# Performance work log

Measured on AMD Instinct MI355X. Metric: run time of the kernel, lower is better.

The kernel has to match this reference:

```python
import jax, jax.numpy as jnp
import numpy as np

D = 1024
B, S = 4, 2048

def setup_inputs() -> dict:
    key = jax.random.key(0)
    ks = jax.random.split(key, 9)
    scale = 1.0 / np.sqrt(D)
    return {
        "queries": jax.random.normal(ks[0], (B, S, D), dtype=jnp.float32),
        "keys": jax.random.normal(ks[1], (B, S, D), dtype=jnp.float32),
        "values": jax.random.normal(ks[2], (B, S, D), dtype=jnp.float32),
        # torch nn.Linear weights: [out, in], y = x @ W.T + b
        "Wq": jax.random.uniform(ks[3], (D, D), jnp.float32, -scale, scale),
        "bq": jax.random.uniform(ks[4], (D,), jnp.float32, -scale, scale),
        "Wk": jax.random.uniform(ks[5], (D, D), jnp.float32, -scale, scale),
        "bk": jax.random.uniform(ks[6], (D,), jnp.float32, -scale, scale),
        "Wv": jax.random.uniform(ks[7], (D, D), jnp.float32, -scale, scale),
        "bv": jax.random.uniform(ks[8], (D,), jnp.float32, -scale, scale),
    }

def reference(queries, keys, values, Wq, bq, Wk, bk, Wv, bv):
    # Linear projections (torch convention: x @ W.T + b)
    Q = jnp.einsum('bsd,ed->bse', queries, Wq) + bq  # [B,S,D]
    K = jnp.einsum('bsd,ed->bse', keys, Wk) + bk
    V = jnp.einsum('bsd,ed->bse', values, Wv) + bv
    # relu attention: no softmax, no scaling (faithful to source)
    scores = jax.nn.relu(jnp.einsum('bqd,bkd->bqk', Q, K))  # [B,S,S]
    return jnp.einsum('bqk,bkd->bqd', scores, V)
```

## Files before the change

### kernel.cpp

```cpp
#include <hip/hip_runtime.h>
#include <hip/hip_bf16.h>
#include <stdint.h>

typedef __bf16 bf16_t;
typedef __bf16 bf16x8 __attribute__((ext_vector_type(8)));
typedef float f32x4 __attribute__((ext_vector_type(4)));

#define TILE 128
#define BK 32

__device__ __forceinline__ void async_copy16(const bf16_t* g, bf16_t* l) {
    __builtin_amdgcn_global_load_lds(
        (const __attribute__((address_space(1))) unsigned int*)(uintptr_t)g,
        (__attribute__((address_space(3))) unsigned int*)(uintptr_t)l,
        16, 0, 0);
}

template<bool OUT_F32, bool RELU, int BIAS_MODE>
__global__ __launch_bounds__(256, 2)
void gemm_bt(const bf16_t* __restrict__ A, const bf16_t* __restrict__ B,
             const float* __restrict__ bias, void* __restrict__ Cp,
             int K, int ldc, long sAb, long sBb, long sCb)
{
    __shared__ bf16_t As[TILE * BK];
    __shared__ bf16_t Bs[TILE * BK];

    const int b      = blockIdx.z;
    const int blockM = blockIdx.y * TILE;
    const int blockN = blockIdx.x * TILE;
    const int t      = threadIdx.x;
    const int lane   = t & 63;
    const int wave   = t >> 6;
    const int wm     = (wave >> 1) * 64;
    const int wn     = (wave & 1) * 64;
    const int fr     = lane & 15;
    const int fk     = (lane >> 4) * 8;
    const int quad   = lane >> 4;

    f32x4 acc[4][4] = {};

    const bf16_t* Ab = A + sAb * (long)b;
    const bf16_t* Bb = B + sBb * (long)b;

    const int c0 = t, c1 = t + 256;
    const int r0 = c0 >> 2, e0 = (c0 & 3) * 8;
    const int r1 = c1 >> 2, e1 = (c1 & 3) * 8;
    const bf16_t* a0 = Ab + (long)(blockM + r0) * K + e0;
    const bf16_t* a1 = Ab + (long)(blockM + r1) * K + e1;
    const bf16_t* b0 = Bb + (long)(blockN + r0) * K + e0;
    const bf16_t* b1 = Bb + (long)(blockN + r1) * K + e1;
    bf16_t* lA0 = &As[c0 * 8]; bf16_t* lA1 = &As[c1 * 8];
    bf16_t* lB0 = &Bs[c0 * 8]; bf16_t* lB1 = &Bs[c1 * 8];

    for (int k0 = 0; k0 < K; k0 += BK) {
        async_copy16(a0 + k0, lA0);
        async_copy16(a1 + k0, lA1);
        async_copy16(b0 + k0, lB0);
        async_copy16(b1 + k0, lB1);
        __syncthreads();

        bf16x8 afr[4], bfr[4];
        #pragma unroll
        for (int i = 0; i < 4; i++)
            afr[i] = *(const bf16x8*)&As[(wm + i*16 + fr) * BK + fk];
        #pragma unroll
        for (int j = 0; j < 4; j++)
            bfr[j] = *(const bf16x8*)&Bs[(wn + j*16 + fr) * BK + fk];

        #pragma unroll
        for (int i = 0; i < 4; i++)
            #pragma unroll
            for (int j = 0; j < 4; j++)
                acc[i][j] = __builtin_amdgcn_mfma_f32_16x16x32_bf16(
                                afr[i], bfr[j], acc[i][j], 0, 0, 0);
        __syncthreads();
    }

    float*  Cf = (float*) Cp + sCb * (long)b;
    bf16_t* Ch = (bf16_t*)Cp + sCb * (long)b;
    #pragma unroll
    for (int i = 0; i < 4; i++) {
        #pragma unroll
        for (int j = 0; j < 4; j++) {
            const int gcol = blockN + wn + j*16 + fr;
            float bcol = 0.f;
            if (BIAS_MODE == 1) bcol = bias[gcol];
            #pragma unroll
            for (int r = 0; r < 4; r++) {
                const int grow = blockM + wm + i*16 + quad*4 + r;
                float vv = acc[i][j][r];
                if (BIAS_MODE == 1) vv += bcol;
                if (BIAS_MODE == 2) vv += bias[grow];
                if (RELU) vv = fmaxf(vv, 0.f);
                if (OUT_F32) Cf[(long)grow * ldc + gcol] = vv;
                else         Ch[(long)grow * ldc + gcol] = (bf16_t)vv;
            }
        }
    }
}

__global__ __launch_bounds__(256)
void cast_all_kernel(const float* __restrict__ q, const float* __restrict__ k,
                     const float* __restrict__ v, const float* __restrict__ Wq,
                     const float* __restrict__ Wk, const float* __restrict__ Wv,
                     bf16_t* __restrict__ ws)
{
    const long BIG = 1048576;
    const long SMALL = 131072;
    long id = (long)blockIdx.x * blockDim.x + threadIdx.x;
    const float* src; bf16_t* dst;
    if (id < 3 * BIG) {
        int s = (int)(id / BIG);
        long off = (id - (long)s * BIG) * 8;
        src = (s == 0 ? q : s == 1 ? k : v) + off;
        dst = ws + (long)s * 8388608 + off;
    } else {
        long id2 = id - 3 * BIG;
        int s = (int)(id2 / SMALL);
        long off = (id2 - (long)s * SMALL) * 8;
        src = (s == 0 ? Wq : s == 1 ? Wk : Wv) + off;
        dst = ws + 25165824L + (long)s * 1048576 + off;
    }
    float4 v0 = ((const float4*)src)[0];
    float4 v1 = ((const float4*)src)[1];
    alignas(16) bf16_t o[8];
    o[0]=(bf16_t)v0.x; o[1]=(bf16_t)v0.y; o[2]=(bf16_t)v0.z; o[3]=(bf16_t)v0.w;
    o[4]=(bf16_t)v1.x; o[5]=(bf16_t)v1.y; o[6]=(bf16_t)v1.z; o[7]=(bf16_t)v1.w;
    *(uint4*)dst = *(const uint4*)o;
}

extern "C" void kernel_launch(void* const* d_in, const int* in_sizes, int n_in,
                              void* d_out, int out_size, void* d_ws, size_t ws_size,
                              hipStream_t stream)
{
    const float* q   = (const float*)d_in[0];
    const float* k   = (const float*)d_in[1];
    const float* v   = (const float*)d_in[2];
    const float* Wq  = (const float*)d_in[3];
    const float* bq  = (const float*)d_in[4];
    const float* Wk  = (const float*)d_in[5];
    const float* bk  = (const float*)d_in[6];
    const float* Wv  = (const float*)d_in[7];
    const float* bv  = (const float*)d_in[8];

    const int B = 4, S = 2048, D = 1024;
    const int BS = B * S;

    bf16_t* ws  = (bf16_t*)d_ws;
    bf16_t* qb  = ws;
    bf16_t* kb  = ws + 8388608L;
    bf16_t* vb  = ws + 16777216L;
    bf16_t* Wqb = ws + 25165824L;
    bf16_t* Wkb = ws + 26214400L;
    bf16_t* Wvb = ws + 27262976L;
    bf16_t* Qp  = ws + 28311552L;
    bf16_t* Kp  = ws + 36700160L;
    bf16_t* VpT = ws + 45088768L;
    bf16_t* Sc  = ws;

    dim3 blk(256);

    cast_all_kernel<<<dim3(13824), blk, 0, stream>>>(q, k, v, Wq, Wk, Wv, ws);

    gemm_bt<false, false, 1><<<dim3(D / TILE, BS / TILE, 1), blk, 0, stream>>>(
        qb, Wqb, bq, Qp, D, D, 0L, 0L, 0L);

    gemm_bt<false, false, 1><<<dim3(D / TILE, BS / TILE, 1), blk, 0, stream>>>(
        kb, Wkb, bk, Kp, D, D, 0L, 0L, 0L);

    gemm_bt<false, false, 2><<<dim3(S / TILE, D / TILE, B), blk, 0, stream>>>(
        Wvb, vb, bv, VpT, D, S, 0L, (long)S * D, (long)D * S);

    gemm_bt<false, true, 0><<<dim3(S / TILE, S / TILE, B), blk, 0, stream>>>(
        Qp, Kp, nullptr, Sc, D, S, (long)S * D, (long)S * D, (long)S * S);

    gemm_bt<false  || true, false, 0><<<dim3(D / TILE, S / TILE, B), blk, 0, stream>>>(
        Sc, VpT, nullptr, d_out, S, D, (long)S * S, (long)D * S, (long)S * D);
}
```

Measured before the change: 332.5 us.

## Use 32x32x16 MFMA, BK=64 with XOR-swizzled LDS, and grouped block order

Rewrites the GEMM inner loop to use 32x32x16 bf16 MFMAs instead of 16x16x32, raising the K tile to 64. LDS chunks are stored with an XOR swizzle to avoid bank conflicts on fragment reads. Block indices are remapped into strips of four column blocks for better L2 reuse. Halving the syncs per K and using larger MFMAs should cut LDS traffic and barrier overhead, at the cost of doubled LDS per block (32 KB), which may reduce occupancy.

```diff
diff --git a/kernel.cpp b/kernel.cpp
--- a/kernel.cpp
+++ b/kernel.cpp
@@ -4,10 +4,10 @@
 
 typedef __bf16 bf16_t;
 typedef __bf16 bf16x8 __attribute__((ext_vector_type(8)));
-typedef float f32x4 __attribute__((ext_vector_type(4)));
+typedef float f32x16 __attribute__((ext_vector_type(16)));
 
 #define TILE 128
-#define BK 32
+#define BK 64
 
 __device__ __forceinline__ void async_copy16(const bf16_t* g, bf16_t* l) {
     __builtin_amdgcn_global_load_lds(
@@ -25,71 +25,90 @@
     __shared__ bf16_t As[TILE * BK];
     __shared__ bf16_t Bs[TILE * BK];
 
-    const int b      = blockIdx.z;
-    const int blockM = blockIdx.y * TILE;
-    const int blockN = blockIdx.x * TILE;
-    const int t      = threadIdx.x;
-    const int lane   = t & 63;
-    const int wave   = t >> 6;
-    const int wm     = (wave >> 1) * 64;
-    const int wn     = (wave & 1) * 64;
-    const int fr     = lane & 15;
-    const int fk     = (lane >> 4) * 8;
-    const int quad   = lane >> 4;
+    const int b  = blockIdx.z;
+    const int nb = gridDim.x, mb = gridDim.y;
+    const int SW = 4;
+    int bid   = blockIdx.y * nb + blockIdx.x;
+    int strip = bid / (mb * SW);
+    int rem   = bid - strip * (mb * SW);
+    int bm    = rem / SW;
+    int bn    = strip * SW + (rem - bm * SW);
+    const int blockM = bm * TILE;
+    const int blockN = bn * TILE;
 
-    f32x4 acc[4][4] = {};
+    const int t    = threadIdx.x;
+    const int lane = t & 63;
+    const int wave = t >> 6;
+    const int wm   = (wave >> 1) * 64;
+    const int wn   = (wave & 1) * 64;
+    const int r32  = lane & 31;
+    const int half = lane >> 5;
+    const int kx   = r32 & 7;
+
+    f32x16 acc[2][2] = {};
 
     const bf16_t* Ab = A + sAb * (long)b;
     const bf16_t* Bb = B + sBb * (long)b;
 
-    const int c0 = t, c1 = t + 256;
-    const int r0 = c0 >> 2, e0 = (c0 & 3) * 8;
-    const int r1 = c1 >> 2, e1 = (c1 & 3) * 8;
-    const bf16_t* a0 = Ab + (long)(blockM + r0) * K + e0;
-    const bf16_t* a1 = Ab + (long)(blockM + r1) * K + e1;
-    const bf16_t* b0 = Bb + (long)(blockN + r0) * K + e0;
-    const bf16_t* b1 = Bb + (long)(blockN + r1) * K + e1;
-    bf16_t* lA0 = &As[c0 * 8]; bf16_t* lA1 = &As[c1 * 8];
-    bf16_t* lB0 = &Bs[c0 * 8]; bf16_t* lB1 = &Bs[c1 * 8];
+    const bf16_t* gA[4]; const bf16_t* gB[4];
+    bf16_t* lA[4]; bf16_t* lB[4];
+    #pragma unroll
+    for (int j = 0; j < 4; j++) {
+        int c   = t + j * 256;
+        int row = c >> 3;
+        int kcl = (c & 7) ^ (row & 7);
+        gA[j] = Ab + (long)(blockM + row) * K + kcl * 8;
+        gB[j] = Bb + (long)(blockN + row) * K + kcl * 8;
+        lA[j] = &As[c * 8];
+        lB[j] = &Bs[c * 8];
+    }
 
     for (int k0 = 0; k0 < K; k0 += BK) {
-        async_copy16(a0 + k0, lA0);
-        async_copy16(a1 + k0, lA1);
-        async_copy16(b0 + k0, lB0);
-        async_copy16(b1 + k0, lB1);
+        #pragma unroll
+        for (int j = 0; j < 4; j++) async_copy16(gA[j] + k0, lA[j]);
+        #pragma unroll
+        for (int j = 0; j < 4; j++) async_copy16(gB[j] + k0, lB[j]);
         __syncthreads();
 
-        bf16x8 afr[4], bfr[4];
         #pragma unroll
-        for (int i = 0; i < 4; i++)
-            afr[i] = *(const bf16x8*)&As[(wm + i*16 + fr) * BK + fk];
-        #pragma unroll
-        for (int j = 0; j < 4; j++)
-            bfr[j] = *(const bf16x8*)&Bs[(wn + j*16 + fr) * BK + fk];
-
-        #pragma unroll
-        for (int i = 0; i < 4; i++)
+        for (int ks = 0; ks < 4; ks++) {
+            const int kc = ks * 2 + half;
+            bf16x8 af[2], bfr[2];
             #pragma unroll
-            for (int j = 0; j < 4; j++)
-                acc[i][j] = __builtin_amdgcn_mfma_f32_16x16x32_bf16(
-                                afr[i], bfr[j], acc[i][j], 0, 0, 0);
+            for (int i = 0; i < 2; i++) {
+                int R = wm + i * 32 + r32;
+                af[i] = *(const bf16x8*)&As[(R * 8 + (kc ^ kx)) * 8];
+            }
+            #pragma unroll
+            for (int j = 0; j < 2; j++) {
+                int C = wn + j * 32 + r32;
+                bfr[j] = *(const bf16x8*)&Bs[(C * 8 + (kc ^ kx)) * 8];
+            }
+            #pragma unroll
+            for (int i = 0; i < 2; i++)
+                #pragma unroll
+                for (int j = 0; j < 2; j++)
+                    acc[i][j] = __builtin_amdgcn_mfma_f32_32x32x16_bf16(
+                                    af[i], bfr[j], acc[i][j], 0, 0, 0);
+        }
         __syncthreads();
     }
 
     float*  Cf = (float*) Cp + sCb * (long)b;
     bf16_t* Ch = (bf16_t*)Cp + sCb * (long)b;
     #pragma unroll
-    for (int i = 0; i < 4; i++) {
+    for (int ti = 0; ti < 2; ti++) {
         #pragma unroll
-        for (int j = 0; j < 4; j++) {
-            const int gcol = blockN + wn + j*16 + fr;
-            float bcol = 0.f;
-            if (BIAS_MODE == 1) bcol = bias[gcol];
+        for (int tj = 0; tj < 2; tj++) {
+            const int gcol = blockN + wn + tj * 32 + r32;
+            float bc = 0.f;
+            if (BIAS_MODE == 1) bc = bias[gcol];
             #pragma unroll
-            for (int r = 0; r < 4; r++) {
-                const int grow = blockM + wm + i*16 + quad*4 + r;
-                float vv = acc[i][j][r];
-                if (BIAS_MODE == 1) vv += bcol;
+            for (int reg = 0; reg < 16; reg++) {
+                const int grow = blockM + wm + ti * 32
+                               + (reg & 3) + 8 * (reg >> 2) + 4 * half;
+                float vv = acc[ti][tj][reg];
+                if (BIAS_MODE == 1) vv += bc;
                 if (BIAS_MODE == 2) vv += bias[grow];
                 if (RELU) vv = fmaxf(vv, 0.f);
                 if (OUT_F32) Cf[(long)grow * ldc + gcol] = vv;
@@ -174,6 +193,6 @@
     gemm_bt<false, true, 0><<<dim3(S / TILE, S / TILE, B), blk, 0, stream>>>(
         Qp, Kp, nullptr, Sc, D, S, (long)S * D, (long)S * D, (long)S * S);
 
-    gemm_bt<false  || true, false, 0><<<dim3(D / TILE, S / TILE, B), blk, 0, stream>>>(
+    gemm_bt<true, false, 0><<<dim3(D / TILE, S / TILE, B), blk, 0, stream>>>(
         Sc, VpT, nullptr, d_out, S, D, (long)S * S, (long)D * S, (long)S * D);
 }
```

Result: faster. 309.9 us (-6.8%).
